# Kernel optimization log

Hardware: AMD Instinct MI355X
Metric: run time of the kernel (lower is better)

Reference implementation:

```python
import jax, jax.numpy as jnp
import numpy as np

B, L, F, H, D, Z, NF = 256, 256, 38, 512, 512, 16, 20
LOG2PI = float(np.log(2.0 * np.pi))


def setup_inputs() -> dict:
    ks = jax.random.split(jax.random.key(0), 32)
    def p(i, shape, s=0.05):
        return jax.random.normal(ks[i], shape, jnp.float32) * s
    return {
        "x": jax.random.normal(ks[0], (B, L, F), jnp.float32),
        "phi_Wih": p(1, (3 * H, F)), "phi_Whh": p(2, (3 * H, H)),
        "phi_bih": p(3, (3 * H,)), "phi_bhh": p(4, (3 * H,)),
        "phi_W1": p(5, (D, H + Z)), "phi_b1": p(6, (D,)),
        "phi_W2": p(7, (D, D)), "phi_b2": p(8, (D,)),
        "zloc_W": p(9, (Z, D)), "zloc_b": p(10, (Z,)),
        "zscale_W": p(11, (Z, D)), "zscale_b": p(12, (Z,)),
        "pu": p(13, (NF, Z)), "pw": p(14, (NF, Z)), "pb": p(15, (NF,)),
        "th_Wih": p(16, (3 * H, Z)), "th_Whh": p(17, (3 * H, H)),
        "th_bih": p(18, (3 * H,)), "th_bhh": p(19, (3 * H,)),
        "th_W1": p(20, (D, H)), "th_b1": p(21, (D,)),
        "th_W2": p(22, (D, D)), "th_b2": p(23, (D,)),
        "xloc_W": p(24, (F, D)), "xloc_b": p(25, (F,)),
        "xscale_W": p(26, (F, D)), "xscale_b": p(27, (F,)),
    }


def _gru(x, h, Wih, Whh, bih, bhh):
    # torch.nn.GRUCell, gate order (r, z, n)
    gi = x @ Wih.T + bih
    gh = h @ Whh.T + bhh
    ir, iz, inn = jnp.split(gi, 3, axis=-1)
    hr, hz, hn = jnp.split(gh, 3, axis=-1)
    r = jax.nn.sigmoid(ir + hr)
    z = jax.nn.sigmoid(iz + hz)
    n = jnp.tanh(inn + r * hn)
    return (1.0 - z) * n + z * h


def _normal_lp(x, loc, scale):
    return -0.5 * ((x - loc) / scale) ** 2 - jnp.log(scale) - 0.5 * LOG2PI


def _forward(x, phi_Wih, phi_Whh, phi_bih, phi_bhh, phi_W1, phi_b1, phi_W2, phi_b2,
             zloc_W, zloc_b, zscale_W, zscale_b, pu, pw, pb,
             th_Wih, th_Whh, th_bih, th_bhh, th_W1, th_b1, th_W2, th_b2,
             xloc_W, xloc_b, xscale_W, xscale_b):
    b, l, f = x.shape
    z_dim = zloc_b.shape[0]
    h_dim = phi_bih.shape[0] // 3
    # fixed rsample noise (reference determinism): z posterior base sample + prior sample
    kz, kp = jax.random.split(jax.random.key(42))
    eps_z = jax.random.normal(kz, (l, b, z_dim), x.dtype)
    eps_p = jax.random.normal(kp, (l, b, z_dim), x.dtype)
    xs = jnp.swapaxes(x, 0, 1)  # [L, B, F]

    # Pyro Planar: u_hat = u + (softplus(w.u) - 1 - w.u) * w / ||w||^2
    wnorm2 = jnp.sum(pw * pw, axis=-1)                     # [NF]
    wu = jnp.sum(pw * pu, axis=-1)                         # [NF]
    uhat = pu + ((jax.nn.softplus(wu) - 1.0 - wu) / wnorm2)[:, None] * pw  # [NF, Z]
    uhat_w = jnp.sum(uhat * pw, axis=-1)                   # [NF]

    def flows(z0):
        def fstep(z, fp):
            w, uh, bb, uw = fp
            a = jnp.tanh(z @ w + bb)                       # [B]
            z_new = z + uh[None, :] * a[:, None]
            ld = jnp.log(jnp.abs(1.0 + (1.0 - a * a) * uw) + 1e-12)  # [B]
            return z_new, ld
        z_fin, lds = jax.lax.scan(fstep, z0, (pw, uhat, pb, uhat_w))
        return z_fin, jnp.sum(lds)

    def step(carry, inp):
        phi_h, th_h, zt, recon, kld = carry
        xt, ez, ep = inp
        phi_h = _gru(xt, phi_h, phi_Wih, phi_Whh, phi_bih, phi_bhh)
        h1 = jax.nn.relu(jnp.concatenate([phi_h, zt], axis=-1) @ phi_W1.T + phi_b1)
        h2 = h1 @ phi_W2.T + phi_b2
        z_loc = h2 @ zloc_W.T + zloc_b
        z_scale = jax.nn.softplus(h2 @ zscale_W.T + zscale_b) + 1e-6
        z0 = z_loc + z_scale * ez
        base_lp = jnp.sum(-0.5 * ez * ez - jnp.log(z_scale) - 0.5 * LOG2PI)
        zt_new, logdet = flows(z0)
        th_h = _gru(zt_new, th_h, th_Wih, th_Whh, th_bih, th_bhh)
        g1 = jax.nn.relu(th_h @ th_W1.T + th_b1)
        g2 = g1 @ th_W2.T + th_b2
        y_loc = g2 @ xloc_W.T + xloc_b
        y_scale = jax.nn.softplus(g2 @ xscale_W.T + xscale_b) + 1e-6
        recon = recon - jnp.sum(_normal_lp(xt, y_loc, y_scale))
        # prior log_prob of its own rsample depends only on eps (loc cancels)
        prior_lp = jnp.sum(-0.5 * ep * ep - 0.5 * LOG2PI)
        kld = kld + (base_lp - logdet) - prior_lp
        return (phi_h, th_h, zt_new, recon, kld), y_loc

    init = (jnp.zeros((b, h_dim), x.dtype), jnp.zeros((b, h_dim), x.dtype),
            jnp.zeros((b, z_dim), x.dtype), jnp.zeros((), x.dtype), jnp.zeros((), x.dtype))
    (_, _, _, recon, kld), y_loc = jax.lax.scan(step, init, (xs, eps_z, eps_p))
    return jnp.swapaxes(y_loc, 0, 1), recon, kld


def reference(x, phi_Wih, phi_Whh, phi_bih, phi_bhh, phi_W1, phi_b1, phi_W2, phi_b2,
              zloc_W, zloc_b, zscale_W, zscale_b, pu, pw, pb,
              th_Wih, th_Whh, th_bih, th_bhh, th_W1, th_b1, th_W2, th_b2,
              xloc_W, xloc_b, xscale_W, xscale_b):
    return _forward(x, phi_Wih, phi_Whh, phi_bih, phi_bhh, phi_W1, phi_b1, phi_W2, phi_b2,
                    zloc_W, zloc_b, zscale_W, zscale_b, pu, pw, pb,
                    th_Wih, th_Whh, th_bih, th_bhh, th_W1, th_b1, th_W2, th_b2,
                    xloc_W, xloc_b, xscale_W, xscale_b)
```

## Files before the change

kernel.cpp:

```cpp
#include <hip/hip_runtime.h>
#include <stdint.h>
#include <math.h>

namespace {

constexpr int B = 256, L = 256, F = 38, H = 512, D = 512, Z = 16, NF = 20;
constexpr float LOG2PI_F = 1.8378770664093453f;
constexpr int LBZ = L * B * Z;
constexpr int HALF = LBZ / 2;
constexpr int HB = H * B;
constexpr int DB = D * B;
constexpr int ZB = Z * B;
constexpr int LFB = L * F * B;


__device__ __forceinline__ float sigmoidf_(float x) {
  return 1.0f / (1.0f + expf(-x));
}
__device__ __forceinline__ float softplusf_(float x) {
  return fmaxf(x, 0.0f) + log1pf(expf(-fabsf(x)));
}

__device__ __forceinline__ void waveReduceAtomicAdd(float* dst, float v, int tid) {
  #pragma unroll
  for (int off = 32; off > 0; off >>= 1) v += __shfl_down(v, off, 64);
  if ((tid & 63) == 0) atomicAdd(dst, v);
}


__host__ __device__ inline uint32_t rotl32_(uint32_t x, int d) {
  return (x << d) | (x >> (32 - d));
}

__host__ __device__ inline void threefry2x32_(uint32_t k0, uint32_t k1,
                                              uint32_t x0, uint32_t x1,
                                              uint32_t& o0, uint32_t& o1) {
  const uint32_t ks2 = k0 ^ k1 ^ 0x1BD11BDAu;
  uint32_t v0 = x0 + k0;
  uint32_t v1 = x1 + k1;
#define TF_RND(r) { v0 += v1; v1 = rotl32_(v1, r); v1 ^= v0; }
  TF_RND(13) TF_RND(15) TF_RND(26) TF_RND(6)
  v0 += k1;  v1 += ks2 + 1u;
  TF_RND(17) TF_RND(29) TF_RND(16) TF_RND(24)
  v0 += ks2; v1 += k0 + 2u;
  TF_RND(13) TF_RND(15) TF_RND(26) TF_RND(6)
  v0 += k0;  v1 += k1 + 3u;
  TF_RND(17) TF_RND(29) TF_RND(16) TF_RND(24)
  v0 += k1;  v1 += ks2 + 4u;
  TF_RND(13) TF_RND(15) TF_RND(26) TF_RND(6)
  v0 += ks2; v1 += k0 + 5u;
#undef TF_RND
  o0 = v0; o1 = v1;
}

__device__ __forceinline__ float erfinv_f_(float x) {
  float w = -log1pf(-x * x);
  float p;
  if (w < 5.0f) {
    w -= 2.5f;
    p = 2.81022636e-08f;
    p = fmaf(p, w, 3.43273939e-07f);
    p = fmaf(p, w, -3.5233877e-06f);
    p = fmaf(p, w, -4.39150654e-06f);
    p = fmaf(p, w, 0.00021858087f);
    p = fmaf(p, w, -0.00125372503f);
    p = fmaf(p, w, -0.00417768164f);
    p = fmaf(p, w, 0.246640727f);
    p = fmaf(p, w, 1.50140941f);
  } else {
    w = sqrtf(w) - 3.0f;
    p = -0.000200214257f;
    p = fmaf(p, w, 0.000100950558f);
    p = fmaf(p, w, 0.00134934322f);
    p = fmaf(p, w, -0.00367342844f);
    p = fmaf(p, w, 0.00573950773f);
    p = fmaf(p, w, -0.0076224613f);
    p = fmaf(p, w, 0.00943887047f);
    p = fmaf(p, w, 1.00167406f);
    p = fmaf(p, w, 2.83297682f);
  }
  return p * x;
}

__device__ __forceinline__ float bits_to_normal_(uint32_t bits) {
  uint32_t m = (bits >> 9) | 0x3f800000u;
  float f = __uint_as_float(m) - 1.0f;
  float u = f * 2.0f + (-0.99999994f);
  u = fmaxf(-0.99999994f, u);
  return 1.41421356f * erfinv_f_(u);
}

__device__ __forceinline__ float flows_dev(float zv[Z], const float* __restrict__ pu,
                                           const float* __restrict__ pw,
                                           const float* __restrict__ pb) {
  float ld = 0.0f;
  for (int f = 0; f < NF; ++f) {
    const float* w = pw + f * Z;
    const float* u = pu + f * Z;
    float wn2 = 0.0f, wu = 0.0f;
    #pragma unroll
    for (int i = 0; i < Z; ++i) { wn2 = fmaf(w[i], w[i], wn2); wu = fmaf(w[i], u[i], wu); }
    float coef = (softplusf_(wu) - 1.0f - wu) / wn2;
    float a_in = pb[f];
    #pragma unroll
    for (int i = 0; i < Z; ++i) a_in = fmaf(zv[i], w[i], a_in);
    float a = tanhf(a_in);
    float uw = 0.0f;
    #pragma unroll
    for (int i = 0; i < Z; ++i) {
      float uh = fmaf(coef, w[i], u[i]);
      uw = fmaf(uh, w[i], uw);
      zv[i] = fmaf(uh, a, zv[i]);
    }
    ld += logf(fabsf(1.0f + (1.0f - a * a) * uw) + 1e-12f);
  }
  return ld;
}


__global__ __launch_bounds__(256) void k_transpose_x(const float* __restrict__ x,
                                                     float* __restrict__ xT) {
  int idx = blockIdx.x * blockDim.x + threadIdx.x;
  int f = idx % F;
  int t = (idx / F) % L;
  int b = idx / (F * L);
  xT[(t * F + f) * B + b] = x[idx];
}

__global__ __launch_bounds__(256) void k_noise(float* __restrict__ eps_z,
                                               float* __restrict__ kld_acc,
                                               uint32_t kz0, uint32_t kz1,
                                               uint32_t kp0, uint32_t kp1) {
  int i = blockIdx.x * blockDim.x + threadIdx.x;
  uint32_t a0, a1, b0, b1;
  threefry2x32_(kz0, kz1, (uint32_t)i, (uint32_t)(i + HALF), a0, a1);
  float ez0 = bits_to_normal_(a0);
  float ez1 = bits_to_normal_(a1);
  eps_z[i] = ez0;
  eps_z[i + HALF] = ez1;
  threefry2x32_(kp0, kp1, (uint32_t)i, (uint32_t)(i + HALF), b0, b1);
  float ep0 = bits_to_normal_(b0);
  float ep1 = bits_to_normal_(b1);
  float local = -0.5f * (ez0 * ez0 + ez1 * ez1) + 0.5f * (ep0 * ep0 + ep1 * ep1);
  waveReduceAtomicAdd(kld_acc, local, threadIdx.x);
}

__global__ void k_finalize(const float* __restrict__ acc, float* __restrict__ out) {
  out[(size_t)B * L * F] = acc[1];
  out[(size_t)B * L * F + 1] = acc[0];
}

__global__ __launch_bounds__(256) void k_compose(
    const float* __restrict__ A, const float* __restrict__ bA,
    const float* __restrict__ W2, const float* __restrict__ b2,
    float* __restrict__ Wc, float* __restrict__ bc) {
  const int r = blockIdx.x;
  const int k = threadIdx.x;
  float acc0 = 0.f, acc1 = 0.f;
  for (int j = 0; j < D; ++j) {
    float a = A[(size_t)r * D + j];
    acc0 = fmaf(a, W2[(size_t)j * D + k], acc0);
    acc1 = fmaf(a, W2[(size_t)j * D + k + 256], acc1);
  }
  Wc[(size_t)r * D + k] = acc0;
  Wc[(size_t)r * D + k + 256] = acc1;
  float accb = 0.f;
  for (int j = k; j < D; j += 256) accb += A[(size_t)r * D + j] * b2[j];
  __shared__ float s[256];
  s[k] = accb;
  __syncthreads();
  for (int off = 128; off > 0; off >>= 1) {
    if (k < off) s[k] += s[k + off];
    __syncthreads();
  }
  if (k == 0) bc[r] = s[0] + bA[r];
}

template<bool THETA>
__device__ __forceinline__ void gru_phase(
    int blk2, const float* __restrict__ xin, const float* __restrict__ hT,
    const float* __restrict__ Wih, const float* __restrict__ Whh,
    const float* __restrict__ bih, const float* __restrict__ bhh,
    float* __restrict__ hout,
    const float* pu, const float* pw, const float* pb, float* kld_acc,
    int w0h, float (&red)[4][4][8][64]) {
  const int tid = threadIdx.x;
  const int lane = tid & 63;
  const int wv = __builtin_amdgcn_readfirstlane(tid >> 6);
  const int j0 = (blk2 >> 2) * 8;
  const int b0 = (blk2 & 3) * 64;
  const int b = b0 + lane;
  constexpr int K1 = THETA ? Z : F;

  float accR[8], accZ[8], accNX[8], accNH[8];
  #pragma unroll
  for (int r = 0; r < 8; ++r) { accR[r] = 0.f; accZ[r] = 0.f; accNX[r] = 0.f; accNH[r] = 0.f; }

  float zv[Z];
  float ld = 0.0f;

  if (wv == 0) {
    const float* wr = Wih + (size_t)(0 * H + j0) * K1;
    const float* wz = Wih + (size_t)(1 * H + j0) * K1;
    const float* wn = Wih + (size_t)(2 * H + j0) * K1;
    if (THETA) {
      #pragma unroll
      for (int i = 0; i < Z; ++i) zv[i] = xin[i * B + b];
      ld = flows_dev(zv, pu, pw, pb);
      #pragma unroll
      for (int k = 0; k < Z; k += 4) {
        #pragma unroll
        for (int r = 0; r < 8; ++r) {
          const float4 w0 = *(const float4*)(wr + r * K1 + k);
          const float4 w1 = *(const float4*)(wz + r * K1 + k);
          const float4 w2 = *(const float4*)(wn + r * K1 + k);
          accR[r]  = fmaf(w0.x, zv[k], fmaf(w0.y, zv[k+1], fmaf(w0.z, zv[k+2], fmaf(w0.w, zv[k+3], accR[r]))));
          accZ[r]  = fmaf(w1.x, zv[k], fmaf(w1.y, zv[k+1], fmaf(w1.z, zv[k+2], fmaf(w1.w, zv[k+3], accZ[r]))));
          accNX[r] = fmaf(w2.x, zv[k], fmaf(w2.y, zv[k+1], fmaf(w2.z, zv[k+2], fmaf(w2.w, zv[k+3], accNX[r]))));
        }
      }
    } else {
      for (int k = 0; k < K1; ++k) {
        float a = xin[k * B + b];
        #pragma unroll
        for (int r = 0; r < 8; ++r) {
          accR[r]  = fmaf(wr[r * K1 + k], a, accR[r]);
          accZ[r]  = fmaf(wz[r * K1 + k], a, accZ[r]);
          accNX[r] = fmaf(wn[r * K1 + k], a, accNX[r]);
        }
      }
    }
  }

  const int rest = (H - w0h) / 3;
  const int hlo = (wv == 0) ? 0 : w0h + (wv - 1) * rest;
  const int hhi = (wv == 0) ? w0h : hlo + rest;
  {
    const float* vr = Whh + (size_t)(0 * H + j0) * H;
    const float* vz = Whh + (size_t)(1 * H + j0) * H;
    const float* vn = Whh + (size_t)(2 * H + j0) * H;
    #pragma unroll 2
    for (int k = hlo; k < hhi; k += 4) {
      const float a0 = hT[(size_t)(k + 0) * B + b];
      const float a1 = hT[(size_t)(k + 1) * B + b];
      const float a2 = hT[(size_t)(k + 2) * B + b];
      const float a3 = hT[(size_t)(k + 3) * B + b];
      #pragma unroll
      for (int r = 0; r < 8; ++r) {
        const float4 w0 = *(const float4*)(vr + (size_t)r * H + k);
        const float4 w1 = *(const float4*)(vz + (size_t)r * H + k);
        const float4 w2 = *(const float4*)(vn + (size_t)r * H + k);
        accR[r]  = fmaf(w0.x, a0, fmaf(w0.y, a1, fmaf(w0.z, a2, fmaf(w0.w, a3, accR[r]))));
        accZ[r]  = fmaf(w1.x, a0, fmaf(w1.y, a1, fmaf(w1.z, a2, fmaf(w1.w, a3, accZ[r]))));
        accNH[r] = fmaf(w2.x, a0, fmaf(w2.y, a1, fmaf(w2.z, a2, fmaf(w2.w, a3, accNH[r]))));
      }
    }
  }

  #pragma unroll
  for (int r = 0; r < 8; ++r) {
    red[wv][0][r][lane] = accR[r];
    red[wv][1][r][lane] = accZ[r];
    red[wv][2][r][lane] = accNX[r];
    red[wv][3][r][lane] = accNH[r];
  }

  if (THETA) {
    if (wv == 0 && j0 == 0) {
      waveReduceAtomicAdd(kld_acc, -ld, lane);
    }
  }

  __syncthreads();

  #pragma unroll
  for (int it = tid; it < 512; it += 256) {
    const int r = it >> 6, l = it & 63;
    float sR = 0.f, sZ = 0.f, sNX = 0.f, sNH = 0.f;
    #pragma unroll
    for (int w = 0; w < 4; ++w) {
      sR  += red[w][0][r][l];
      sZ  += red[w][1][r][l];
      sNX += red[w][2][r][l];
      sNH += red[w][3][r][l];
    }
    const int j = j0 + r;
    const int bb = b0 + l;
    const float rg = sigmoidf_(sR + bih[j] + bhh[j]);
    const float zg = sigmoidf_(sZ + bih[H + j] + bhh[H + j]);
    const float ng = tanhf(sNX + bih[2 * H + j] + rg * (sNH + bhh[2 * H + j]));
    const float hp = hT[(size_t)j * B + bb];
    hout[(size_t)j * B + bb] = (1.0f - zg) * ng + zg * hp;
  }
}

__device__ __forceinline__ void lin8_phase(
    int blk2, const float* __restrict__ A1, int K1v,
    const float* __restrict__ W, const float* __restrict__ bias,
    float* __restrict__ outp, int relu, float* shbase) {
  const int tid = threadIdx.x;
  const int lane = tid & 63;
  const int wv = __builtin_amdgcn_readfirstlane(tid >> 6);
  const int r0 = (blk2 >> 2) * 8;
  const int b0 = (blk2 & 3) * 64;
  const int b = b0 + lane;
  const int Kv = K1v;
  const int klo = wv * (Kv >> 2);
  const int khi = klo + (Kv >> 2);

  float acc[8];
  #pragma unroll
  for (int r = 0; r < 8; ++r) acc[r] = 0.f;

  const float* wbase = W + (size_t)r0 * Kv;
  #pragma unroll 4
  for (int k = klo; k < khi; k += 4) {
    const float a0 = A1[(size_t)(k + 0) * B + b];
    const float a1 = A1[(size_t)(k + 1) * B + b];
    const float a2 = A1[(size_t)(k + 2) * B + b];
    const float a3 = A1[(size_t)(k + 3) * B + b];
    #pragma unroll
    for (int r = 0; r < 8; ++r) {
      const float4 w4 = *(const float4*)(wbase + (size_t)r * Kv + k);
      acc[r] = fmaf(w4.x, a0, fmaf(w4.y, a1, fmaf(w4.z, a2, fmaf(w4.w, a3, acc[r]))));
    }
  }

  float* red = shbase;
  #pragma unroll
  for (int r = 0; r < 8; ++r) red[(wv * 8 + r) * 64 + lane] = acc[r];
  __syncthreads();

  #pragma unroll
  for (int it = tid; it < 512; it += 256) {
    int r = it >> 6, l = it & 63;
    float s = red[(0 * 8 + r) * 64 + l] + red[(1 * 8 + r) * 64 + l]
            + red[(2 * 8 + r) * 64 + l] + red[(3 * 8 + r) * 64 + l] + bias[r0 + r];
    if (relu) s = fmaxf(s, 0.f);
    outp[(size_t)(r0 + r) * B + b0 + l] = s;
  }
}

__device__ __forceinline__ void mlp1_phi_phase(
    int blk2, const float* __restrict__ hphiT, const float* __restrict__ z0prev,
    const float* __restrict__ W, const float* __restrict__ bias,
    float* __restrict__ h1T,
    const float* pu, const float* pw, const float* pb, float* shbase) {
  const int tid = threadIdx.x;
  const int lane = tid & 63;
  const int wv = __builtin_amdgcn_readfirstlane(tid >> 6);
  const int r0 = (blk2 >> 2) * 8;
  const int b0 = (blk2 & 3) * 64;
  const int b = b0 + lane;
  constexpr int Kv = H + Z;
  const int klo = wv * 140;
  const int khi = (wv == 3) ? H : klo + 140;

  float acc[8];
  #pragma unroll
  for (int r = 0; r < 8; ++r) acc[r] = 0.f;

  const float* wbase = W + (size_t)r0 * Kv;
  #pragma unroll 4
  for (int k = klo; k < khi; k += 4) {
    const float a0 = hphiT[(size_t)(k + 0) * B + b];
    const float a1 = hphiT[(size_t)(k + 1) * B + b];
    const float a2 = hphiT[(size_t)(k + 2) * B + b];
    const float a3 = hphiT[(size_t)(k + 3) * B + b];
    #pragma unroll
    for (int r = 0; r < 8; ++r) {
      const float4 w4 = *(const float4*)(wbase + (size_t)r * Kv + k);
      acc[r] = fmaf(w4.x, a0, fmaf(w4.y, a1, fmaf(w4.z, a2, fmaf(w4.w, a3, acc[r]))));
    }
  }
  if (wv == 3 && z0prev != nullptr) {
    float zv[Z];
    #pragma unroll
    for (int i = 0; i < Z; ++i) zv[i] = z0prev[i * B + b];
    flows_dev(zv, pu, pw, pb);
    #pragma unroll
    for (int i = 0; i < Z; i += 4) {
      #pragma unroll
      for (int r = 0; r < 8; ++r) {
        const float4 w4 = *(const float4*)(wbase + (size_t)r * Kv + H + i);
        acc[r] = fmaf(w4.x, zv[i], fmaf(w4.y, zv[i+1], fmaf(w4.z, zv[i+2], fmaf(w4.w, zv[i+3], acc[r]))));
      }
    }
  }

  float* red = shbase;
  #pragma unroll
  for (int r = 0; r < 8; ++r) red[(wv * 8 + r) * 64 + lane] = acc[r];
  __syncthreads();

  #pragma unroll
  for (int it = tid; it < 512; it += 256) {
    int r = it >> 6, l = it & 63;
    float s = red[(0 * 8 + r) * 64 + l] + red[(1 * 8 + r) * 64 + l]
            + red[(2 * 8 + r) * 64 + l] + red[(3 * 8 + r) * 64 + l] + bias[r0 + r];
    s = fmaxf(s, 0.f);
    h1T[(size_t)(r0 + r) * B + b0 + l] = s;
  }
}

__device__ __forceinline__ void zhead_phase(
    int blk2, const float* __restrict__ h1T,
    const float* __restrict__ Wzl, const float* __restrict__ bzl,
    const float* __restrict__ Wzs, const float* __restrict__ bzs,
    const float* __restrict__ eps_t, float* __restrict__ z0T,
    float* kld_acc, float* shbase) {
  const int tid = threadIdx.x;
  const int lane = tid & 63;
  const int wv = __builtin_amdgcn_readfirstlane(tid >> 6);
  const int z0q = (blk2 >> 2) * 4;
  const int b0 = (blk2 & 3) * 64;
  const int b = b0 + lane;
  const int klo = wv * (D >> 2), khi = klo + (D >> 2);

  const float* wp[8];
  #pragma unroll
  for (int i = 0; i < 8; ++i) {
    int zz = z0q + (i >> 1);
    wp[i] = ((i & 1) ? Wzs : Wzl) + (size_t)zz * D;
  }
  float acc[8];
  #pragma unroll
  for (int i = 0; i < 8; ++i) acc[i] = 0.f;
  #pragma unroll 4
  for (int k = klo; k < khi; k += 4) {
    const float a0 = h1T[(size_t)(k + 0) * B + b];
    const float a1 = h1T[(size_t)(k + 1) * B + b];
    const float a2 = h1T[(size_t)(k + 2) * B + b];
    const float a3 = h1T[(size_t)(k + 3) * B + b];
    #pragma unroll
    for (int i = 0; i < 8; ++i) {
      const float4 w4 = *(const float4*)(wp[i] + k);
      acc[i] = fmaf(w4.x, a0, fmaf(w4.y, a1, fmaf(w4.z, a2, fmaf(w4.w, a3, acc[i]))));
    }
  }

  float* red = shbase;
  #pragma unroll
  for (int i = 0; i < 8; ++i) red[(wv * 8 + i) * 64 + lane] = acc[i];
  __syncthreads();

  int zi = tid >> 6, l = tid & 63;
  int zz = z0q + zi;
  int bb = b0 + l;
  float sl = red[(0 * 8 + 2 * zi) * 64 + l] + red[(1 * 8 + 2 * zi) * 64 + l]
           + red[(2 * 8 + 2 * zi) * 64 + l] + red[(3 * 8 + 2 * zi) * 64 + l] + bzl[zz];
  float ss = red[(0 * 8 + 2 * zi + 1) * 64 + l] + red[(1 * 8 + 2 * zi + 1) * 64 + l]
           + red[(2 * 8 + 2 * zi + 1) * 64 + l] + red[(3 * 8 + 2 * zi + 1) * 64 + l] + bzs[zz];
  float scale = softplusf_(ss) + 1e-6f;
  float ez = eps_t[bb * Z + zz];
  z0T[zz * B + bb] = sl + scale * ez;
  waveReduceAtomicAdd(kld_acc, -logf(scale), tid);
}

__device__ __forceinline__ void yhead_phase(
    int blk2, int t, const float* __restrict__ g1T,
    const float* __restrict__ Wyl, const float* __restrict__ byl,
    const float* __restrict__ Wys, const float* __restrict__ bys,
    const float* __restrict__ xT, float* __restrict__ out_yloc,
    float* recon_acc, float* shbase) {
  const int tid = threadIdx.x;
  const int lane = tid & 63;
  const int wv = __builtin_amdgcn_readfirstlane(tid >> 6);
  const int f0 = (blk2 >> 2) * 4;
  const int b0 = (blk2 & 3) * 64;
  const int b = b0 + lane;
  const int klo = wv * (D >> 2), khi = klo + (D >> 2);

  const float* wp[8];
  #pragma unroll
  for (int i = 0; i < 8; ++i) {
    int ff = f0 + (i >> 1);
    int fc = ff < F ? ff : 0;
    wp[i] = ((i & 1) ? Wys : Wyl) + (size_t)fc * D;
  }
  float acc[8];
  #pragma unroll
  for (int i = 0; i < 8; ++i) acc[i] = 0.f;
  #pragma unroll 4
  for (int k = klo; k < khi; k += 4) {
    const float a0 = g1T[(size_t)(k + 0) * B + b];
    const float a1 = g1T[(size_t)(k + 1) * B + b];
    const float a2 = g1T[(size_t)(k + 2) * B + b];
    const float a3 = g1T[(size_t)(k + 3) * B + b];
    #pragma unroll
    for (int i = 0; i < 8; ++i) {
      const float4 w4 = *(const float4*)(wp[i] + k);
      acc[i] = fmaf(w4.x, a0, fmaf(w4.y, a1, fmaf(w4.z, a2, fmaf(w4.w, a3, acc[i]))));
    }
  }

  float* red = shbase;
  #pragma unroll
  for (int i = 0; i < 8; ++i) red[(wv * 8 + i) * 64 + lane] = acc[i];
  __syncthreads();

  int fi = tid >> 6, l = tid & 63;
  int ff = f0 + fi;
  int bb = b0 + l;
  float nl = 0.0f;
  if (ff < F) {
    float loc = red[(0 * 8 + 2 * fi) * 64 + l] + red[(1 * 8 + 2 * fi) * 64 + l]
              + red[(2 * 8 + 2 * fi) * 64 + l] + red[(3 * 8 + 2 * fi) * 64 + l] + byl[ff];
    float sp = red[(0 * 8 + 2 * fi + 1) * 64 + l] + red[(1 * 8 + 2 * fi + 1) * 64 + l]
             + red[(2 * 8 + 2 * fi + 1) * 64 + l] + red[(3 * 8 + 2 * fi + 1) * 64 + l] + bys[ff];
    float scale = softplusf_(sp) + 1e-6f;
    out_yloc[((size_t)bb * L + t) * F + ff] = loc;
    float xv = xT[((size_t)t * F + ff) * B + bb];
    float d = (xv - loc) / scale;
    nl = 0.5f * d * d + logf(scale) + 0.5f * LOG2PI_F;
  }
  waveReduceAtomicAdd(recon_acc, nl, tid);
}

struct CW {
  const float *phi_Wih, *phi_Whh, *phi_bih, *phi_bhh, *phi_W1, *phi_b1;
  const float *th_Wih, *th_Whh, *th_bih, *th_bhh, *th_W1, *th_b1;
  const float *Wzl, *bzl, *Wzs, *bzs, *Wyl, *byl, *Wys, *bys;
  const float *pu, *pw, *pb, *xT;
  float *acc, *out, *h1T, *g1T;
};

__global__ __launch_bounds__(256) void kA(
    CW C, const float* xt, const float* phi_c, float* phi_n,
    const float* z0_in, const float* th_c, float* th_n,
    float* z0_out, const float* eps_t, int t_y,
    int hasPhi, int hasTh, int hasZ, int hasY) {
  __shared__ float red[4][4][8][64];
  float* sh = &red[0][0][0][0];
  const int blk = blockIdx.x;
  if (blk < 256) {
    if (hasPhi)
      gru_phase<false>(blk, xt, phi_c, C.phi_Wih, C.phi_Whh, C.phi_bih, C.phi_bhh,
                       phi_n, nullptr, nullptr, nullptr, nullptr, 104, red);
  } else if (blk < 512) {
    if (hasTh)
      gru_phase<true>(blk - 256, z0_in, th_c, C.th_Wih, C.th_Whh, C.th_bih, C.th_bhh,
                      th_n, C.pu, C.pw, C.pb, C.acc, 56, red);
  } else if (blk < 528) {
    if (hasZ)
      zhead_phase(blk - 512, C.h1T, C.Wzl, C.bzl, C.Wzs, C.bzs, eps_t, z0_out,
                  C.acc, sh);
  } else {
    if (hasY)
      yhead_phase(blk - 528, t_y, C.g1T, C.Wyl, C.byl, C.Wys, C.bys, C.xT,
                  C.out, C.acc + 1, sh);
  }
}

__global__ __launch_bounds__(256) void kB(
    CW C, const float* phiT, const float* z0prev, const float* thT,
    int hasPhiM, int hasThM) {
  __shared__ float red[4 * 8 * 64];
  const int blk = blockIdx.x;
  if (blk < 256) {
    if (hasPhiM)
      mlp1_phi_phase(blk, phiT, z0prev, C.phi_W1, C.phi_b1, C.h1T,
                     C.pu, C.pw, C.pb, red);
  } else {
    if (hasThM)
      lin8_phase(blk - 256, thT, H, C.th_W1, C.th_b1, C.g1T, 1, red);
  }
}

}

extern "C" void kernel_launch(void* const* d_in, const int* in_sizes, int n_in,
                              void* d_out, int out_size, void* d_ws, size_t ws_size,
                              hipStream_t stream) {
  const float* x        = (const float*)d_in[0];
  const float* phi_Wih  = (const float*)d_in[1];
  const float* phi_Whh  = (const float*)d_in[2];
  const float* phi_bih  = (const float*)d_in[3];
  const float* phi_bhh  = (const float*)d_in[4];
  const float* phi_W1   = (const float*)d_in[5];
  const float* phi_b1   = (const float*)d_in[6];
  const float* phi_W2   = (const float*)d_in[7];
  const float* phi_b2   = (const float*)d_in[8];
  const float* zloc_W   = (const float*)d_in[9];
  const float* zloc_b   = (const float*)d_in[10];
  const float* zscale_W = (const float*)d_in[11];
  const float* zscale_b = (const float*)d_in[12];
  const float* pu       = (const float*)d_in[13];
  const float* pw       = (const float*)d_in[14];
  const float* pb       = (const float*)d_in[15];
  const float* th_Wih   = (const float*)d_in[16];
  const float* th_Whh   = (const float*)d_in[17];
  const float* th_bih   = (const float*)d_in[18];
  const float* th_bhh   = (const float*)d_in[19];
  const float* th_W1    = (const float*)d_in[20];
  const float* th_b1    = (const float*)d_in[21];
  const float* th_W2    = (const float*)d_in[22];
  const float* th_b2    = (const float*)d_in[23];
  const float* xloc_W   = (const float*)d_in[24];
  const float* xloc_b   = (const float*)d_in[25];
  const float* xscale_W = (const float*)d_in[26];
  const float* xscale_b = (const float*)d_in[27];

  float* out = (float*)d_out;
  float* ws = (float*)d_ws;

  float* acc   = ws;
  float* eps_z = ws + 64;
  float* xT    = eps_z + LBZ;
  float* phi0  = xT + LFB;
  float* phi1  = phi0 + HB;
  float* th0   = phi1 + HB;
  float* th1   = th0 + HB;
  float* z0a   = th1 + HB;
  float* z0b   = z0a + ZB;
  float* h1T   = z0b + ZB;
  float* g1T   = h1T + DB;
  float* Wzl   = g1T + DB;
  float* Wzs   = Wzl + Z * D;
  float* bzl   = Wzs + Z * D;
  float* bzs   = bzl + 64;
  float* Wyl   = bzs + 64;
  float* Wys   = Wyl + F * D;
  float* byl   = Wys + F * D;
  float* bys   = byl + 64;

  float* phibuf[2] = {phi0, phi1};
  float* thbuf[2]  = {th0, th1};
  float* z0buf[2]  = {z0a, z0b};

  hipMemsetAsync(acc, 0, 64 * sizeof(float), stream);
  hipMemsetAsync(phi0, 0, (size_t)HB * sizeof(float), stream);
  hipMemsetAsync(th1, 0, (size_t)HB * sizeof(float), stream);

  uint32_t a0, a1, b0, b1;
  threefry2x32_(0u, 42u, 0u, 2u, a0, a1);
  threefry2x32_(0u, 42u, 1u, 3u, b0, b1);
  const uint32_t kz0 = a0, kz1 = b0, kp0 = a1, kp1 = b1;

  k_transpose_x<<<(B * L * F) / 256, 256, 0, stream>>>(x, xT);
  k_noise<<<HALF / 256, 256, 0, stream>>>(eps_z, acc, kz0, kz1, kp0, kp1);

  k_compose<<<Z, 256, 0, stream>>>(zloc_W, zloc_b, phi_W2, phi_b2, Wzl, bzl);
  k_compose<<<Z, 256, 0, stream>>>(zscale_W, zscale_b, phi_W2, phi_b2, Wzs, bzs);
  k_compose<<<F, 256, 0, stream>>>(xloc_W, xloc_b, th_W2, th_b2, Wyl, byl);
  k_compose<<<F, 256, 0, stream>>>(xscale_W, xscale_b, th_W2, th_b2, Wys, bys);

  CW C;
  C.phi_Wih = phi_Wih; C.phi_Whh = phi_Whh; C.phi_bih = phi_bih; C.phi_bhh = phi_bhh;
  C.phi_W1 = phi_W1; C.phi_b1 = phi_b1;
  C.th_Wih = th_Wih; C.th_Whh = th_Whh; C.th_bih = th_bih; C.th_bhh = th_bhh;
  C.th_W1 = th_W1; C.th_b1 = th_b1;
  C.Wzl = Wzl; C.bzl = bzl; C.Wzs = Wzs; C.bzs = bzs;
  C.Wyl = Wyl; C.byl = byl; C.Wys = Wys; C.bys = bys;
  C.pu = pu; C.pw = pw; C.pb = pb; C.xT = xT;
  C.acc = acc; C.out = out; C.h1T = h1T; C.g1T = g1T;

  for (int i = 0; i <= L + 2; ++i) {
    const int hasPhi = (i < L);
    const int hasTh  = (i >= 2 && i <= L + 1);
    const int hasZ   = (i >= 1 && i <= L);
    const int hasY   = (i >= 3);

    const float* xt     = xT + (size_t)(hasPhi ? i : 0) * F * B;
    const float* phi_c  = phibuf[i & 1];
    float*       phi_n  = phibuf[(i + 1) & 1];
    const float* z0_in  = z0buf[i & 1];
    const float* th_c   = thbuf[(i + 1) & 1];
    float*       th_n   = thbuf[i & 1];
    float*       z0_out = z0buf[(i + 1) & 1];
    const float* eps_t  = eps_z + (size_t)(hasZ ? (i - 1) : 0) * B * Z;
    const int    t_y    = hasY ? (i - 3) : 0;

    kA<<<568, 256, 0, stream>>>(C, xt, phi_c, phi_n, z0_in, th_c, th_n,
                                z0_out, eps_t, t_y, hasPhi, hasTh, hasZ, hasY);

    const int hasPhiM = (i < L);
    const int hasThM  = (i >= 2 && i <= L + 1);
    if (hasPhiM || hasThM) {
      const float* phiT   = phibuf[(i + 1) & 1];
      const float* z0prev = (i >= 1) ? z0buf[(i + 1) & 1]
                                     : nullptr;
      const float* thT    = thbuf[i & 1];
      kB<<<512, 256, 0, stream>>>(C, phiT, z0prev, thT, hasPhiM, hasThM);
    }
  }

  k_finalize<<<1, 1, 0, stream>>>(acc, out);
}
```

Measured before the change: 27.38 ms.

## Replace per-step kernel launches with persistent kernel and hierarchical grid barrier

Roughly 516 kernel launches across the recurrent time loop are replaced by a single persistent 512-block kernel. It moves between phases using a three-level atomic grid barrier, with relaxed agent-scope atomic loads and stores for cross-block data. The z/y head blocks now run on the first 56 phi-GRU blocks after those blocks finish their GRU work. The goal is to remove launch overhead and implicit kernel boundaries per step. The risks are that correctness depends on all 512 blocks being co-resident, that the atomic loads may be slower than plain cached loads, and that the head work is serialized inside some blocks.

```diff
diff --git a/kernel.cpp b/kernel.cpp
--- a/kernel.cpp
+++ b/kernel.cpp
@@ -12,6 +12,14 @@
 constexpr int DB = D * B;
 constexpr int ZB = Z * B;
 constexpr int LFB = L * F * B;
+constexpr int GRIDN = 512;
+
+__device__ __forceinline__ float aload_(const float* p) {
+  return __hip_atomic_load(p, __ATOMIC_RELAXED, __HIP_MEMORY_SCOPE_AGENT);
+}
+__device__ __forceinline__ void astore_(float* p, float v) {
+  __hip_atomic_store(p, v, __ATOMIC_RELAXED, __HIP_MEMORY_SCOPE_AGENT);
+}
 
 
 __device__ __forceinline__ float sigmoidf_(float x) {
@@ -25,6 +33,28 @@
   #pragma unroll
   for (int off = 32; off > 0; off >>= 1) v += __shfl_down(v, off, 64);
   if ((tid & 63) == 0) atomicAdd(dst, v);
+}
+
+__device__ __forceinline__ void gsync_(uint32_t* bar, int blk, uint32_t n) {
+  __syncthreads();
+  if (threadIdx.x == 0) {
+    const uint32_t tgt = 8u * n - 1u;
+    uint32_t o1 = __hip_atomic_fetch_add(&bar[192 + ((blk >> 3) << 4)], 1u,
+                                         __ATOMIC_RELEASE, __HIP_MEMORY_SCOPE_AGENT);
+    if (o1 == tgt) {
+      uint32_t o2 = __hip_atomic_fetch_add(&bar[32 + ((blk >> 6) << 4)], 1u,
+                                           __ATOMIC_RELEASE, __HIP_MEMORY_SCOPE_AGENT);
+      if (o2 == tgt) {
+        uint32_t o3 = __hip_atomic_fetch_add(&bar[16], 1u,
+                                             __ATOMIC_RELEASE, __HIP_MEMORY_SCOPE_AGENT);
+        if (o3 == tgt)
+          __hip_atomic_store(&bar[0], n, __ATOMIC_RELEASE, __HIP_MEMORY_SCOPE_AGENT);
+      }
+    }
+    while (__hip_atomic_load(&bar[0], __ATOMIC_RELAXED, __HIP_MEMORY_SCOPE_AGENT) < n)
+      __builtin_amdgcn_s_sleep(1);
+  }
+  __syncthreads();
 }
 
 
@@ -205,7 +235,7 @@
     const float* wn = Wih + (size_t)(2 * H + j0) * K1;
     if (THETA) {
       #pragma unroll
-      for (int i = 0; i < Z; ++i) zv[i] = xin[i * B + b];
+      for (int i = 0; i < Z; ++i) zv[i] = aload_(xin + i * B + b);
       ld = flows_dev(zv, pu, pw, pb);
       #pragma unroll
       for (int k = 0; k < Z; k += 4) {
@@ -241,10 +271,10 @@
     const float* vn = Whh + (size_t)(2 * H + j0) * H;
     #pragma unroll 2
     for (int k = hlo; k < hhi; k += 4) {
-      const float a0 = hT[(size_t)(k + 0) * B + b];
-      const float a1 = hT[(size_t)(k + 1) * B + b];
-      const float a2 = hT[(size_t)(k + 2) * B + b];
-      const float a3 = hT[(size_t)(k + 3) * B + b];
+      const float a0 = aload_(hT + (size_t)(k + 0) * B + b);
+      const float a1 = aload_(hT + (size_t)(k + 1) * B + b);
+      const float a2 = aload_(hT + (size_t)(k + 2) * B + b);
+      const float a3 = aload_(hT + (size_t)(k + 3) * B + b);
       #pragma unroll
       for (int r = 0; r < 8; ++r) {
         const float4 w0 = *(const float4*)(vr + (size_t)r * H + k);
@@ -289,8 +319,8 @@
     const float rg = sigmoidf_(sR + bih[j] + bhh[j]);
     const float zg = sigmoidf_(sZ + bih[H + j] + bhh[H + j]);
     const float ng = tanhf(sNX + bih[2 * H + j] + rg * (sNH + bhh[2 * H + j]));
-    const float hp = hT[(size_t)j * B + bb];
-    hout[(size_t)j * B + bb] = (1.0f - zg) * ng + zg * hp;
+    const float hp = aload_(hT + (size_t)j * B + bb);
+    astore_(hout + (size_t)j * B + bb, (1.0f - zg) * ng + zg * hp);
   }
 }
 
@@ -315,10 +345,10 @@
   const float* wbase = W + (size_t)r0 * Kv;
   #pragma unroll 4
   for (int k = klo; k < khi; k += 4) {
-    const float a0 = A1[(size_t)(k + 0) * B + b];
-    const float a1 = A1[(size_t)(k + 1) * B + b];
-    const float a2 = A1[(size_t)(k + 2) * B + b];
-    const float a3 = A1[(size_t)(k + 3) * B + b];
+    const float a0 = aload_(A1 + (size_t)(k + 0) * B + b);
+    const float a1 = aload_(A1 + (size_t)(k + 1) * B + b);
+    const float a2 = aload_(A1 + (size_t)(k + 2) * B + b);
+    const float a3 = aload_(A1 + (size_t)(k + 3) * B + b);
     #pragma unroll
     for (int r = 0; r < 8; ++r) {
       const float4 w4 = *(const float4*)(wbase + (size_t)r * Kv + k);
@@ -337,7 +367,7 @@
     float s = red[(0 * 8 + r) * 64 + l] + red[(1 * 8 + r) * 64 + l]
             + red[(2 * 8 + r) * 64 + l] + red[(3 * 8 + r) * 64 + l] + bias[r0 + r];
     if (relu) s = fmaxf(s, 0.f);
-    outp[(size_t)(r0 + r) * B + b0 + l] = s;
+    astore_(outp + (size_t)(r0 + r) * B + b0 + l, s);
   }
 }
 
@@ -363,10 +393,10 @@
   const float* wbase = W + (size_t)r0 * Kv;
   #pragma unroll 4
   for (int k = klo; k < khi; k += 4) {
-    const float a0 = hphiT[(size_t)(k + 0) * B + b];
-    const float a1 = hphiT[(size_t)(k + 1) * B + b];
-    const float a2 = hphiT[(size_t)(k + 2) * B + b];
-    const float a3 = hphiT[(size_t)(k + 3) * B + b];
+    const float a0 = aload_(hphiT + (size_t)(k + 0) * B + b);
+    const float a1 = aload_(hphiT + (size_t)(k + 1) * B + b);
+    const float a2 = aload_(hphiT + (size_t)(k + 2) * B + b);
+    const float a3 = aload_(hphiT + (size_t)(k + 3) * B + b);
     #pragma unroll
     for (int r = 0; r < 8; ++r) {
       const float4 w4 = *(const float4*)(wbase + (size_t)r * Kv + k);
@@ -376,7 +406,7 @@
   if (wv == 3 && z0prev != nullptr) {
     float zv[Z];
     #pragma unroll
-    for (int i = 0; i < Z; ++i) zv[i] = z0prev[i * B + b];
+    for (int i = 0; i < Z; ++i) zv[i] = aload_(z0prev + i * B + b);
     flows_dev(zv, pu, pw, pb);
     #pragma unroll
     for (int i = 0; i < Z; i += 4) {
@@ -399,7 +429,7 @@
     float s = red[(0 * 8 + r) * 64 + l] + red[(1 * 8 + r) * 64 + l]
             + red[(2 * 8 + r) * 64 + l] + red[(3 * 8 + r) * 64 + l] + bias[r0 + r];
     s = fmaxf(s, 0.f);
-    h1T[(size_t)(r0 + r) * B + b0 + l] = s;
+    astore_(h1T + (size_t)(r0 + r) * B + b0 + l, s);
   }
 }
 
@@ -428,10 +458,10 @@
   for (int i = 0; i < 8; ++i) acc[i] = 0.f;
   #pragma unroll 4
   for (int k = klo; k < khi; k += 4) {
-    const float a0 = h1T[(size_t)(k + 0) * B + b];
-    const float a1 = h1T[(size_t)(k + 1) * B + b];
-    const float a2 = h1T[(size_t)(k + 2) * B + b];
-    const float a3 = h1T[(size_t)(k + 3) * B + b];
+    const float a0 = aload_(h1T + (size_t)(k + 0) * B + b);
+    const float a1 = aload_(h1T + (size_t)(k + 1) * B + b);
+    const float a2 = aload_(h1T + (size_t)(k + 2) * B + b);
+    const float a3 = aload_(h1T + (size_t)(k + 3) * B + b);
     #pragma unroll
     for (int i = 0; i < 8; ++i) {
       const float4 w4 = *(const float4*)(wp[i] + k);
@@ -453,7 +483,7 @@
            + red[(2 * 8 + 2 * zi + 1) * 64 + l] + red[(3 * 8 + 2 * zi + 1) * 64 + l] + bzs[zz];
   float scale = softplusf_(ss) + 1e-6f;
   float ez = eps_t[bb * Z + zz];
-  z0T[zz * B + bb] = sl + scale * ez;
+  astore_(z0T + zz * B + bb, sl + scale * ez);
   waveReduceAtomicAdd(kld_acc, -logf(scale), tid);
 }
 
@@ -483,10 +513,10 @@
   for (int i = 0; i < 8; ++i) acc[i] = 0.f;
   #pragma unroll 4
   for (int k = klo; k < khi; k += 4) {
-    const float a0 = g1T[(size_t)(k + 0) * B + b];
-    const float a1 = g1T[(size_t)(k + 1) * B + b];
-    const float a2 = g1T[(size_t)(k + 2) * B + b];
-    const float a3 = g1T[(size_t)(k + 3) * B + b];
+    const float a0 = aload_(g1T + (size_t)(k + 0) * B + b);
+    const float a1 = aload_(g1T + (size_t)(k + 1) * B + b);
+    const float a2 = aload_(g1T + (size_t)(k + 2) * B + b);
+    const float a3 = aload_(g1T + (size_t)(k + 3) * B + b);
     #pragma unroll
     for (int i = 0; i < 8; ++i) {
       const float4 w4 = *(const float4*)(wp[i] + k);
@@ -517,53 +547,69 @@
   waveReduceAtomicAdd(recon_acc, nl, tid);
 }
 
-struct CW {
+struct PP {
+  const float *xT, *eps_z;
   const float *phi_Wih, *phi_Whh, *phi_bih, *phi_bhh, *phi_W1, *phi_b1;
   const float *th_Wih, *th_Whh, *th_bih, *th_bhh, *th_W1, *th_b1;
   const float *Wzl, *bzl, *Wzs, *bzs, *Wyl, *byl, *Wys, *bys;
-  const float *pu, *pw, *pb, *xT;
-  float *acc, *out, *h1T, *g1T;
+  const float *pu, *pw, *pb;
+  float *phi0, *phi1, *th0, *th1, *z0a, *z0b, *h1T, *g1T, *acc, *out;
+  uint32_t* bar;
 };
 
-__global__ __launch_bounds__(256) void kA(
-    CW C, const float* xt, const float* phi_c, float* phi_n,
-    const float* z0_in, const float* th_c, float* th_n,
-    float* z0_out, const float* eps_t, int t_y,
-    int hasPhi, int hasTh, int hasZ, int hasY) {
+__global__ __launch_bounds__(256, 2) void k_persist(PP P) {
   __shared__ float red[4][4][8][64];
   float* sh = &red[0][0][0][0];
   const int blk = blockIdx.x;
-  if (blk < 256) {
-    if (hasPhi)
-      gru_phase<false>(blk, xt, phi_c, C.phi_Wih, C.phi_Whh, C.phi_bih, C.phi_bhh,
-                       phi_n, nullptr, nullptr, nullptr, nullptr, 104, red);
-  } else if (blk < 512) {
-    if (hasTh)
-      gru_phase<true>(blk - 256, z0_in, th_c, C.th_Wih, C.th_Whh, C.th_bih, C.th_bhh,
-                      th_n, C.pu, C.pw, C.pb, C.acc, 56, red);
-  } else if (blk < 528) {
-    if (hasZ)
-      zhead_phase(blk - 512, C.h1T, C.Wzl, C.bzl, C.Wzs, C.bzs, eps_t, z0_out,
-                  C.acc, sh);
-  } else {
-    if (hasY)
-      yhead_phase(blk - 528, t_y, C.g1T, C.Wyl, C.byl, C.Wys, C.bys, C.xT,
-                  C.out, C.acc + 1, sh);
-  }
-}
-
-__global__ __launch_bounds__(256) void kB(
-    CW C, const float* phiT, const float* z0prev, const float* thT,
-    int hasPhiM, int hasThM) {
-  __shared__ float red[4 * 8 * 64];
-  const int blk = blockIdx.x;
-  if (blk < 256) {
-    if (hasPhiM)
-      mlp1_phi_phase(blk, phiT, z0prev, C.phi_W1, C.phi_b1, C.h1T,
-                     C.pu, C.pw, C.pb, red);
-  } else {
-    if (hasThM)
-      lin8_phase(blk - 256, thT, H, C.th_W1, C.th_b1, C.g1T, 1, red);
+  uint32_t n = 0;
+
+  for (int i = 0; i <= L + 2; ++i) {
+    const bool hasPhi = (i < L);
+    const bool hasTh  = (i >= 2 && i <= L + 1);
+    const bool hasZ   = (i >= 1 && i <= L);
+    const bool hasY   = (i >= 3);
+
+    const float* xt     = P.xT + (size_t)(hasPhi ? i : 0) * F * B;
+    const float* phi_c  = (i & 1) ? P.phi1 : P.phi0;
+    float*       phi_n  = (i & 1) ? P.phi0 : P.phi1;
+    const float* z0_in  = (i & 1) ? P.z0b : P.z0a;
+    const float* th_c   = (i & 1) ? P.th0 : P.th1;
+    float*       th_n   = (i & 1) ? P.th1 : P.th0;
+    float*       z0_out = (i & 1) ? P.z0a : P.z0b;
+
+    if (blk < 256) {
+      if (hasPhi)
+        gru_phase<false>(blk, xt, phi_c, P.phi_Wih, P.phi_Whh, P.phi_bih,
+                         P.phi_bhh, phi_n, nullptr, nullptr, nullptr, nullptr,
+                         104, red);
+      if (blk < 56) {
+        __syncthreads();
+        if (blk < 16) {
+          if (hasZ)
+            zhead_phase(blk, P.h1T, P.Wzl, P.bzl, P.Wzs, P.bzs,
+                        P.eps_z + (size_t)(i - 1) * B * Z, z0_out, P.acc, sh);
+        } else {
+          if (hasY)
+            yhead_phase(blk - 16, i - 3, P.g1T, P.Wyl, P.byl, P.Wys, P.bys,
+                        P.xT, P.out, P.acc + 1, sh);
+        }
+      }
+    } else {
+      if (hasTh)
+        gru_phase<true>(blk - 256, z0_in, th_c, P.th_Wih, P.th_Whh, P.th_bih,
+                        P.th_bhh, th_n, P.pu, P.pw, P.pb, P.acc, 56, red);
+    }
+    ++n; gsync_(P.bar, blk, n);
+
+    if (blk < 256) {
+      if (hasPhi)
+        mlp1_phi_phase(blk, phi_n, (i >= 1) ? z0_out : nullptr,
+                       P.phi_W1, P.phi_b1, P.h1T, P.pu, P.pw, P.pb, sh);
+    } else {
+      if (hasTh)
+        lin8_phase(blk - 256, th_n, H, P.th_W1, P.th_b1, P.g1T, 1, sh);
+    }
+    ++n; gsync_(P.bar, blk, n);
   }
 }
 
@@ -605,7 +651,8 @@
   float* ws = (float*)d_ws;
 
   float* acc   = ws;
-  float* eps_z = ws + 64;
+  uint32_t* bar = (uint32_t*)(ws + 64);
+  float* eps_z = ws + 64 + 2048;
   float* xT    = eps_z + LBZ;
   float* phi0  = xT + LFB;
   float* phi1  = phi0 + HB;
@@ -624,11 +671,7 @@
   float* byl   = Wys + F * D;
   float* bys   = byl + 64;
 
-  float* phibuf[2] = {phi0, phi1};
-  float* thbuf[2]  = {th0, th1};
-  float* z0buf[2]  = {z0a, z0b};
-
-  hipMemsetAsync(acc, 0, 64 * sizeof(float), stream);
+  hipMemsetAsync(ws, 0, (64 + 2048) * sizeof(float), stream);
   hipMemsetAsync(phi0, 0, (size_t)HB * sizeof(float), stream);
   hipMemsetAsync(th1, 0, (size_t)HB * sizeof(float), stream);
 
@@ -645,45 +688,20 @@
   k_compose<<<F, 256, 0, stream>>>(xloc_W, xloc_b, th_W2, th_b2, Wyl, byl);
   k_compose<<<F, 256, 0, stream>>>(xscale_W, xscale_b, th_W2, th_b2, Wys, bys);
 
-  CW C;
-  C.phi_Wih = phi_Wih; C.phi_Whh = phi_Whh; C.phi_bih = phi_bih; C.phi_bhh = phi_bhh;
-  C.phi_W1 = phi_W1; C.phi_b1 = phi_b1;
-  C.th_Wih = th_Wih; C.th_Whh = th_Whh; C.th_bih = th_bih; C.th_bhh = th_bhh;
-  C.th_W1 = th_W1; C.th_b1 = th_b1;
-  C.Wzl = Wzl; C.bzl = bzl; C.Wzs = Wzs; C.bzs = bzs;
-  C.Wyl = Wyl; C.byl = byl; C.Wys = Wys; C.bys = bys;
-  C.pu = pu; C.pw = pw; C.pb = pb; C.xT = xT;
-  C.acc = acc; C.out = out; C.h1T = h1T; C.g1T = g1T;
-
-  for (int i = 0; i <= L + 2; ++i) {
-    const int hasPhi = (i < L);
-    const int hasTh  = (i >= 2 && i <= L + 1);
-    const int hasZ   = (i >= 1 && i <= L);
-    const int hasY   = (i >= 3);
-
-    const float* xt     = xT + (size_t)(hasPhi ? i : 0) * F * B;
-    const float* phi_c  = phibuf[i & 1];
-    float*       phi_n  = phibuf[(i + 1) & 1];
-    const float* z0_in  = z0buf[i & 1];
-    const float* th_c   = thbuf[(i + 1) & 1];
-    float*       th_n   = thbuf[i & 1];
-    float*       z0_out = z0buf[(i + 1) & 1];
-    const float* eps_t  = eps_z + (size_t)(hasZ ? (i - 1) : 0) * B * Z;
-    const int    t_y    = hasY ? (i - 3) : 0;
-
-    kA<<<568, 256, 0, stream>>>(C, xt, phi_c, phi_n, z0_in, th_c, th_n,
-                                z0_out, eps_t, t_y, hasPhi, hasTh, hasZ, hasY);
-
-    const int hasPhiM = (i < L);
-    const int hasThM  = (i >= 2 && i <= L + 1);
-    if (hasPhiM || hasThM) {
-      const float* phiT   = phibuf[(i + 1) & 1];
-      const float* z0prev = (i >= 1) ? z0buf[(i + 1) & 1]
-                                     : nullptr;
-      const float* thT    = thbuf[i & 1];
-      kB<<<512, 256, 0, stream>>>(C, phiT, z0prev, thT, hasPhiM, hasThM);
-    }
-  }
+  PP P;
+  P.xT = xT; P.eps_z = eps_z;
+  P.phi_Wih = phi_Wih; P.phi_Whh = phi_Whh; P.phi_bih = phi_bih; P.phi_bhh = phi_bhh;
+  P.phi_W1 = phi_W1; P.phi_b1 = phi_b1;
+  P.th_Wih = th_Wih; P.th_Whh = th_Whh; P.th_bih = th_bih; P.th_bhh = th_bhh;
+  P.th_W1 = th_W1; P.th_b1 = th_b1;
+  P.Wzl = Wzl; P.bzl = bzl; P.Wzs = Wzs; P.bzs = bzs;
+  P.Wyl = Wyl; P.byl = byl; P.Wys = Wys; P.bys = bys;
+  P.pu = pu; P.pw = pw; P.pb = pb;
+  P.phi0 = phi0; P.phi1 = phi1; P.th0 = th0; P.th1 = th1;
+  P.z0a = z0a; P.z0b = z0b; P.h1T = h1T; P.g1T = g1T;
+  P.acc = acc; P.out = out; P.bar = (uint32_t*)bar;
+
+  k_persist<<<GRIDN, 256, 0, stream>>>(P);
 
   k_finalize<<<1, 1, 0, stream>>>(acc, out);
 }
```

Result: slower. 35.72 ms (+30.5%).
